# Optimization experiments

Measured on AMD Instinct MI355X. Metric: run time of the kernel, lower is better.

## Reference

```python
import jax, jax.numpy as jnp
import numpy as np

LMAX_IN = 3
LMAX_OUT = 3
C = 64          # num_channel
H = 64          # num_channel_hidden
N_NODES = 2048
N_EDGES = 8192

# All coupled (l1, l2, l3) paths with |l1-l2| <= l3 <= min(l1+l2, lmax_out)
COMBS = [(l1, l2, l3)
         for l1 in range(LMAX_IN + 1)
         for l2 in range(LMAX_OUT + 1)
         for l3 in range(abs(l1 - l2), min(l1 + l2, LMAX_OUT) + 1)]
COUNTS = {l3: sum(1 for c in COMBS if c[2] == l3) for l3 in range(LMAX_OUT + 1)}

# Fixed coupling (Clebsch-Gordan-like) tensors for each path, shape (2l1+1, 2l2+1, 2l3+1).
# Deterministic constants (not trained / not differentiated), standing in for the
# e3nn CG coefficients used by InterEinsumTC.
_rng = np.random.RandomState(1234)
CG = [jnp.asarray((_rng.randn(2 * l1 + 1, 2 * l2 + 1, 2 * l3 + 1) * 0.2).astype(np.float32))
      for (l1, l2, l3) in COMBS]


def setup_inputs() -> dict:
    key = jax.random.key(0)
    ks = jax.random.split(key, 16)
    inp = {}
    for l in range(LMAX_OUT + 1):
        inp[f"x{l}"] = jax.random.normal(ks[l], (N_NODES, C, 2 * l + 1), dtype=jnp.float32)
        inp[f"y{l}"] = jax.random.normal(ks[4 + l], (N_EDGES, 2 * l + 1), dtype=jnp.float32)
        fan_in = C * COUNTS[l]
        inp[f"w_lin{l}"] = jax.random.normal(ks[8 + l], (fan_in, H), dtype=jnp.float32) / np.float32(np.sqrt(fan_in))
    inp["ws"] = jax.random.normal(ks[12], (N_EDGES, C * len(COMBS)), dtype=jnp.float32)
    inp["edge_index"] = jax.random.randint(ks[13], (2, N_EDGES), 0, N_NODES, dtype=jnp.int32)
    return inp


def _forward(x0, x1, x2, x3, y0, y1, y2, y3, ws, w_lin0, w_lin1, w_lin2, w_lin3, edge_index):
    xs = (x0, x1, x2, x3)
    ys = (y0, y1, y2, y3)
    wl = (w_lin0, w_lin1, w_lin2, w_lin3)
    src, dst = edge_index[0], edge_index[1]
    # per-edge gather of node features for every input degree
    xg = [x[src] for x in xs]                      # [E, C, 2l1+1]
    buf = {l3: [] for l3 in range(LMAX_OUT + 1)}
    for i, (l1, l2, l3) in enumerate(COMBS):
        # tensor-product contraction: [E, C, 2l3+1]
        out = jnp.einsum('lmn,ecl,em->ecn', CG[i], xg[l1], ys[l2])
        w = ws[:, i * C:(i + 1) * C][:, :, None]   # [E, C, 1] per-path per-channel weight
        buf[l3].append(w * out)
    res = []
    for l3 in range(LMAX_OUT + 1):
        m_ji = jnp.concatenate(buf[l3], axis=1)    # [E, C*count_l3, 2l3+1]
        m_i = jax.ops.segment_sum(m_ji, dst, num_segments=N_NODES)  # scatter-sum -> [N, C*count, 2l3+1]
        res.append(jnp.einsum('ncm,ch->nhm', m_i, wl[l3]))          # per-l3 linear -> [N, H, 2l3+1]
    return tuple(res)


def reference(x0, x1, x2, x3, y0, y1, y2, y3, ws, w_lin0, w_lin1, w_lin2, w_lin3, edge_index):
    return _forward(x0, x1, x2, x3, y0, y1, y2, y3, ws,
                    w_lin0, w_lin1, w_lin2, w_lin3, edge_index)
```

## Files before the change

kernel.cpp:

```cpp
#include <hip/hip_runtime.h>
#include <hip/hip_bf16.h>
#include <cmath>
#include <cstdint>

#define NNODES 2048
#define NEDGES 8192
#define NCH 64
#define NHID 64
#define NPATH 34
#define NTASK (NPATH * NCH)
#define CGTOT 3436
#define MROW 9984
#define TTOT2 888
#define EBLK 8

#define MI_BYTES ((size_t)NNODES * MROW * 2)
#define XT_BYTES ((size_t)NNODES * 16 * NCH * 2)
#define OFF_OFF  (MI_BYTES)
#define CUR_OFF  (OFF_OFF + 2052 * 4)
#define PACK_OFF (CUR_OFF + 2048 * 4)
#define ORD_OFF  (PACK_OFF + 8192 * 4)
#define XT_OFF   (ORD_OFF + 2048 * 4)
#define CGP_OFF  (XT_OFF + XT_BYTES)
#define CGP_FLOATS (TTOT2 * 9)

typedef __attribute__((ext_vector_type(8))) short short8;
typedef __attribute__((ext_vector_type(4))) float floatx4;

struct PathTables {
  int l1[NPATH], l2[NPATH], l3[NPATH];
  int cg_off[NPATH], t_off2[NPATH], rank[NPATH];
  int gpaths[2][20], gnp[2], gbase[2], glen[2];
  int cg_total, ttot2, npaths;
};

constexpr PathTables make_tables() {
  PathTables tb{};
  int np = 0;
  for (int a = 0; a < 4; ++a)
    for (int b = 0; b < 4; ++b) {
      int lo = a > b ? a - b : b - a;
      int hi = a + b < 3 ? a + b : 3;
      for (int c = lo; c <= hi; ++c) { tb.l1[np] = a; tb.l2[np] = b; tb.l3[np] = c; ++np; }
    }
  int cg = 0;
  int cnt[4] = {0, 0, 0, 0};
  for (int i = 0; i < np; ++i) {
    tb.cg_off[i] = cg; tb.rank[i] = cnt[tb.l3[i]]++;
    cg += (2 * tb.l1[i] + 1) * (2 * tb.l2[i] + 1) * (2 * tb.l3[i] + 1);
  }
  int tt2 = 0;
  for (int g = 0; g < 2; ++g) {
    tb.gbase[g] = tt2;
    for (int i = 0; i < np; ++i) {
      int gi = (tb.l3[i] == 0 || tb.l3[i] == 3) ? 0 : 1;
      if (gi != g) continue;
      tb.gpaths[g][tb.gnp[g]++] = i;
      tb.t_off2[i] = tt2;
      int d1 = 2 * tb.l1[i] + 1, d3 = 2 * tb.l3[i] + 1;
      tt2 += ((d1 * d3 + 7) / 8) * 8;
    }
    tb.glen[g] = tt2 - tb.gbase[g];
  }
  tb.cg_total = cg; tb.ttot2 = tt2; tb.npaths = np;
  return tb;
}

constexpr PathTables H_TB = make_tables();
static_assert(H_TB.npaths == NPATH, "npaths");
static_assert(H_TB.cg_total == CGTOT, "cgtot");
static_assert(H_TB.ttot2 == TTOT2, "ttot2");
static_assert(H_TB.gnp[0] == 14 && H_TB.gnp[1] == 20, "gnp");
static_assert(H_TB.gbase[1] == 432 && H_TB.glen[1] == 456, "gsplit");

__constant__ PathTables d_tb = make_tables();

namespace {
struct MT19937 {
  uint32_t mt[624]; int mti; bool has_g; double gval;
  void seed(uint32_t s) {
    for (int i = 0; i < 624; ++i) { mt[i] = s; s = 1812433253u * (s ^ (s >> 30)) + (uint32_t)i + 1u; }
    mti = 624; has_g = false; gval = 0.0;
  }
  uint32_t next() {
    if (mti >= 624) {
      for (int i = 0; i < 624; ++i) {
        uint32_t y = (mt[i] & 0x80000000u) | (mt[(i + 1) % 624] & 0x7fffffffu);
        mt[i] = mt[(i + 397) % 624] ^ (y >> 1) ^ ((y & 1u) ? 0x9908b0dfu : 0u);
      }
      mti = 0;
    }
    uint32_t y = mt[mti++];
    y ^= y >> 11; y ^= (y << 7) & 0x9d2c5680u; y ^= (y << 15) & 0xefc60000u; y ^= y >> 18;
    return y;
  }
  double rdbl() {
    uint32_t a = next() >> 5, b = next() >> 6;
    return ((double)a * 67108864.0 + (double)b) / 9007199254740992.0;
  }
  double gauss() {
    if (has_g) { has_g = false; return gval; }
    double x1, x2, r2;
    do {
      x1 = 2.0 * rdbl() - 1.0;
      x2 = 2.0 * rdbl() - 1.0;
      r2 = x1 * x1 + x2 * x2;
    } while (r2 >= 1.0 || r2 == 0.0);
    double f = std::sqrt(-2.0 * std::log(r2) / r2);
    gval = f * x1; has_g = true;
    return f * x2;
  }
};

float host_pack[CGP_FLOATS];
float* g_cg_dev = nullptr;
bool g_cg_ok = false;

struct CGInit {
  CGInit() {
    static float cg[CGTOT];
    MT19937 g; g.seed(1234u);
    int idx = 0;
    for (int i = 0; i < NPATH; ++i) {
      int d1 = 2 * H_TB.l1[i] + 1, d2 = 2 * H_TB.l2[i] + 1, d3 = 2 * H_TB.l3[i] + 1;
      int sz = d1 * d2 * d3;
      for (int k = 0; k < sz; ++k) cg[idx++] = (float)(g.gauss() * 0.2);
    }
    const int ybase[4] = {0, 1, 4, 9};
    for (int k = 0; k < CGP_FLOATS; ++k) host_pack[k] = 0.f;
    for (int i = 0; i < NPATH; ++i) {
      int d1 = 2 * H_TB.l1[i] + 1, d2 = 2 * H_TB.l2[i] + 1, d3 = 2 * H_TB.l3[i] + 1;
      for (int l = 0; l < d1; ++l)
        for (int n3 = 0; n3 < d3; ++n3) {
          int tt2 = H_TB.t_off2[i] + l * d3 + n3;
          for (int m = 0; m < d2; ++m)
            host_pack[tt2 * 8 + m] = cg[H_TB.cg_off[i] + l * d2 * d3 + m * d3 + n3];
          host_pack[TTOT2 * 8 + tt2] = (float)ybase[H_TB.l2[i]];
        }
    }
    (void)hipHostRegister(host_pack, sizeof(host_pack), hipHostRegisterDefault);
    void* p = nullptr;
    if (hipMalloc(&p, sizeof(host_pack)) == hipSuccess && p) {
      if (hipMemcpy(p, host_pack, sizeof(host_pack), hipMemcpyHostToDevice) == hipSuccess) {
        float back = -1.f;
        if (hipMemcpy(&back, (float*)p + (CGP_FLOATS - 1), sizeof(float),
                      hipMemcpyDeviceToHost) == hipSuccess && back == host_pack[CGP_FLOATS - 1]) {
          g_cg_dev = (float*)p;
          g_cg_ok = true;
        }
      }
    }
  }
} cg_init_instance;
}

__device__ __forceinline__ float bf2f(unsigned short u) {
  union { unsigned int i; float f; } v; v.i = ((unsigned int)u) << 16; return v.f;
}
__device__ __forceinline__ unsigned short f2bf(float f) {
  __hip_bfloat16 h = __float2bfloat16(f);
  union { __hip_bfloat16 h; unsigned short u; } v; v.h = h; return v.u;
}

__global__ __launch_bounds__(1024) void scan_kernel(
    const int* __restrict__ edge_index, int* __restrict__ off, int* __restrict__ cursor,
    int* __restrict__ order)
{
  __shared__ int ldeg[NNODES];
  __shared__ int csum[1024];
  __shared__ int hist[64];
  const int t = threadIdx.x;
  for (int i = t; i < NNODES; i += 1024) ldeg[i] = 0;
  __syncthreads();
  const int* __restrict__ dsts = edge_index + NEDGES;
  for (int e = t; e < NEDGES; e += 1024) atomicAdd(&ldeg[dsts[e]], 1);
  __syncthreads();
  const int l0 = ldeg[2 * t], l1 = ldeg[2 * t + 1];
  const int s = l0 + l1;
  csum[t] = s;
  __syncthreads();
  for (int o = 1; o < 1024; o <<= 1) {
    int v = (t >= o) ? csum[t - o] : 0;
    __syncthreads();
    csum[t] += v;
    __syncthreads();
  }
  int run = csum[t] - s;
  off[2 * t] = run; cursor[2 * t] = run;
  off[2 * t + 1] = run + l0; cursor[2 * t + 1] = run + l0;
  if (t == 0) off[NNODES] = NEDGES;
  if (t < 64) hist[t] = 0;
  __syncthreads();
  for (int i = t; i < NNODES; i += 1024) {
    int d = ldeg[i]; d = d > 63 ? 63 : d;
    atomicAdd(&hist[63 - d], 1);
  }
  __syncthreads();
  if (t == 0) { int r2 = 0; for (int b = 0; b < 64; ++b) { int c = hist[b]; hist[b] = r2; r2 += c; } }
  __syncthreads();
  for (int i = t; i < NNODES; i += 1024) {
    int d = ldeg[i]; d = d > 63 ? 63 : d;
    int pos = atomicAdd(&hist[63 - d], 1);
    order[pos] = i;
  }
}

__global__ __launch_bounds__(256) void fill_xt_kernel(
    const int* __restrict__ edge_index, int* __restrict__ cursor, int* __restrict__ pack,
    const float* __restrict__ x0, const float* __restrict__ x1,
    const float* __restrict__ x2, const float* __restrict__ x3,
    __hip_bfloat16* __restrict__ xT)
{
  const int b = blockIdx.x;
  const int t = threadIdx.x;
  if (b < 32) {
    const int e = b * 256 + t;
    const int d = edge_index[NEDGES + e];
    const int s = edge_index[e];
    const int pos = atomicAdd(&cursor[d], 1);
    pack[pos] = e | (s << 13);
  } else {
    const int n = b - 32;
    for (int idx = t; idx < 1024; idx += 256) {
      const int j = idx >> 6, c = idx & 63;
      const float* src; int d1, m;
      if (j < 1)      { src = x0; d1 = 1; m = j; }
      else if (j < 4) { src = x1; d1 = 3; m = j - 1; }
      else if (j < 9) { src = x2; d1 = 5; m = j - 4; }
      else            { src = x3; d1 = 7; m = j - 9; }
      const float v = src[((size_t)n * NCH + c) * d1 + m];
      xT[((size_t)n * 16 + j) * NCH + c] = __float2bfloat16(v);
    }
  }
}

template <int D1, int D3>
__device__ __forceinline__ void tp_task_run(
    int wcol, int toff_l, int rank, int nb, const int* __restrict__ epk,
    const float (*Ts)[456], const float* __restrict__ ws,
    const unsigned short* __restrict__ xT,
    int n, bool first, __hip_bfloat16* __restrict__ m_out)
{
  constexpr int Kc = (D3 == 1) ? 256 : (D3 == 3) ? 576 : (D3 == 5) ? 704 : 640;
  constexpr int Rc = (D3 == 1) ? 0 : (D3 == 3) ? 256 : (D3 == 5) ? 1984 : 5504;
  constexpr int JB = (D1 == 1) ? 0 : (D1 == 3) ? 1 : (D1 == 5) ? 4 : 9;
  const int c = wcol & 63;

  float wv_[EBLK];
#pragma unroll
  for (int ei = 0; ei < EBLK; ++ei)
    wv_[ei] = (ei < nb) ? ws[(size_t)(epk[ei] & 8191) * NTASK + wcol] : 0.f;

  float acc[D3];
#pragma unroll
  for (int m = 0; m < D3; ++m) acc[m] = 0.f;

  for (int ei = 0; ei < nb; ++ei) {
    const int s = epk[ei] >> 13;
    const unsigned short* __restrict__ xr = xT + ((size_t)s * 16 + JB) * NCH + c;
    const float* __restrict__ Tp = &Ts[ei][toff_l];
    float u[D3];
#pragma unroll
    for (int m = 0; m < D3; ++m) u[m] = 0.f;
#pragma unroll
    for (int l = 0; l < D1; ++l) {
      const float xv = bf2f(xr[l * NCH]);
#pragma unroll
      for (int m = 0; m < D3; ++m) u[m] += xv * Tp[l * D3 + m];
    }
#pragma unroll
    for (int m = 0; m < D3; ++m) acc[m] += wv_[ei] * u[m];
  }

  __hip_bfloat16* mo = m_out + (size_t)n * MROW + Rc + rank * NCH + c;
  if (first) {
#pragma unroll
    for (int m = 0; m < D3; ++m) mo[m * Kc] = __float2bfloat16(acc[m]);
  } else {
#pragma unroll
    for (int m = 0; m < D3; ++m)
      mo[m * Kc] = __float2bfloat16(__bfloat162float(mo[m * Kc]) + acc[m]);
  }
}

__global__ __launch_bounds__(256) void tp_node_kernel(
    const float* __restrict__ y0, const float* __restrict__ y1,
    const float* __restrict__ y2, const float* __restrict__ y3,
    const float* __restrict__ ws, const unsigned short* __restrict__ xT,
    const float* __restrict__ cg_pack,
    const int* __restrict__ off, const int* __restrict__ pack,
    const int* __restrict__ order,
    __hip_bfloat16* __restrict__ m_out)
{
  __shared__ float Ts[EBLK][456];
  __shared__ float y_s[EBLK][18];
  __shared__ int epk[EBLK];

  const int bid = blockIdx.x;
  const int n = order[bid >> 1];
  const int g = bid & 1;
  const int t = threadIdx.x;
  const int beg = off[n];
  const int cnt = off[n + 1] - beg;
  const int gbase = d_tb.gbase[g];
  const int glen  = d_tb.glen[g];
  const int ntask = d_tb.gnp[g] << 6;
  const float* __restrict__ metaf = cg_pack + TTOT2 * 8;

  for (int base = 0; base == 0 || base < cnt; base += EBLK) {
    int nb = cnt - base;
    nb = nb < 0 ? 0 : (nb > EBLK ? EBLK : nb);
    if (t < nb) epk[t] = pack[beg + base + t];
    if (t >= 64 && t < 64 + 2 * EBLK) y_s[(t - 64) >> 1][16 + (t & 1)] = 0.f;
    __syncthreads();
    if (t < nb * 16) {
      const int ei = t >> 4, j = t & 15;
      const int e = epk[ei] & 8191;
      float v;
      if (j < 1)      v = y0[e];
      else if (j < 4) v = y1[e * 3 + (j - 1)];
      else if (j < 9) v = y2[e * 5 + (j - 4)];
      else            v = y3[e * 7 + (j - 9)];
      y_s[ei][j] = v;
    }
    __syncthreads();
    for (int ei = 0; ei < nb; ++ei) {
      for (int j = t; j < glen; j += 256) {
        const int tt2 = gbase + j;
        const float4 a = *(const float4*)(cg_pack + tt2 * 8);
        const float4 c4 = *(const float4*)(cg_pack + tt2 * 8 + 4);
        const int yb = (int)metaf[tt2];
        const float* yy = &y_s[ei][yb];
        Ts[ei][j] = a.x * yy[0] + a.y * yy[1] + a.z * yy[2] + a.w * yy[3]
                  + c4.x * yy[4] + c4.y * yy[5] + c4.z * yy[6] + c4.w * yy[7];
      }
    }
    __syncthreads();

    const bool first = (base == 0);
    for (int k = 0; k * 256 + t < ntask; ++k) {
      const int tl = k * 256 + t;
      const int i = d_tb.gpaths[g][tl >> 6];
      const int wcol = (i << 6) | (tl & 63);
      const int toff_l = d_tb.t_off2[i] - gbase;
      const int rk = d_tb.rank[i];
      const int code = d_tb.l1[i] * 4 + d_tb.l3[i];
      switch (code) {
        case  0: tp_task_run<1,1>(wcol, toff_l, rk, nb, epk, Ts, ws, xT, n, first, m_out); break;
        case  1: tp_task_run<1,3>(wcol, toff_l, rk, nb, epk, Ts, ws, xT, n, first, m_out); break;
        case  2: tp_task_run<1,5>(wcol, toff_l, rk, nb, epk, Ts, ws, xT, n, first, m_out); break;
        case  3: tp_task_run<1,7>(wcol, toff_l, rk, nb, epk, Ts, ws, xT, n, first, m_out); break;
        case  4: tp_task_run<3,1>(wcol, toff_l, rk, nb, epk, Ts, ws, xT, n, first, m_out); break;
        case  5: tp_task_run<3,3>(wcol, toff_l, rk, nb, epk, Ts, ws, xT, n, first, m_out); break;
        case  6: tp_task_run<3,5>(wcol, toff_l, rk, nb, epk, Ts, ws, xT, n, first, m_out); break;
        case  7: tp_task_run<3,7>(wcol, toff_l, rk, nb, epk, Ts, ws, xT, n, first, m_out); break;
        case  8: tp_task_run<5,1>(wcol, toff_l, rk, nb, epk, Ts, ws, xT, n, first, m_out); break;
        case  9: tp_task_run<5,3>(wcol, toff_l, rk, nb, epk, Ts, ws, xT, n, first, m_out); break;
        case 10: tp_task_run<5,5>(wcol, toff_l, rk, nb, epk, Ts, ws, xT, n, first, m_out); break;
        case 11: tp_task_run<5,7>(wcol, toff_l, rk, nb, epk, Ts, ws, xT, n, first, m_out); break;
        case 12: tp_task_run<7,1>(wcol, toff_l, rk, nb, epk, Ts, ws, xT, n, first, m_out); break;
        case 13: tp_task_run<7,3>(wcol, toff_l, rk, nb, epk, Ts, ws, xT, n, first, m_out); break;
        case 14: tp_task_run<7,5>(wcol, toff_l, rk, nb, epk, Ts, ws, xT, n, first, m_out); break;
        default: tp_task_run<7,7>(wcol, toff_l, rk, nb, epk, Ts, ws, xT, n, first, m_out); break;
      }
    }
    __syncthreads();
  }
}

template <int D3, int K, int ROFF>
__device__ __forceinline__ void lin_mfma_body(
    int blk, const unsigned short* __restrict__ mu, const float* __restrict__ wl,
    float* __restrict__ out, unsigned short (*A_s)[72], unsigned short (*W_s)[72])
{
  const int t = threadIdx.x;
  const int wv = t >> 6;
  const int lane = t & 63;
  const int idx16 = lane & 15;
  const int quad = lane >> 4;
  const int r0 = blk * 64;

  floatx4 acc[4] = {{0.f,0.f,0.f,0.f},{0.f,0.f,0.f,0.f},{0.f,0.f,0.f,0.f},{0.f,0.f,0.f,0.f}};

  for (int k0 = 0; k0 < K; k0 += 64) {
    for (int idx = t; idx < 512; idx += 256) {
      const int rr = idx >> 3, ck = (idx & 7) * 8;
      const int r = r0 + rr;
      const int nn = r / D3, mm = r - nn * D3;
      const uint4 v = *(const uint4*)(mu + (size_t)nn * MROW + ROFF + mm * K + k0 + ck);
      *(uint4*)&A_s[rr][ck] = v;
    }
    {
      const int h = t & 63, kg = t >> 6;
      unsigned short tmp[16];
#pragma unroll
      for (int j = 0; j < 16; ++j)
        tmp[j] = f2bf(wl[(size_t)(k0 + kg * 16 + j) * 64 + h]);
      *(uint4*)&W_s[h][kg * 16]     = *(const uint4*)&tmp[0];
      *(uint4*)&W_s[h][kg * 16 + 8] = *(const uint4*)&tmp[8];
    }
    __syncthreads();
#pragma unroll
    for (int ks = 0; ks < 2; ++ks) {
      const int kb = ks * 32 + quad * 8;
      const short8 af = *(const short8*)&A_s[wv * 16 + idx16][kb];
#pragma unroll
      for (int nt = 0; nt < 4; ++nt) {
        const short8 bf = *(const short8*)&W_s[nt * 16 + idx16][kb];
        acc[nt] = __builtin_amdgcn_mfma_f32_16x16x32_bf16(af, bf, acc[nt], 0, 0, 0);
      }
    }
    __syncthreads();
  }

#pragma unroll
  for (int nt = 0; nt < 4; ++nt) {
    const int h = nt * 16 + idx16;
#pragma unroll
    for (int r = 0; r < 4; ++r) {
      const int row = r0 + wv * 16 + quad * 4 + r;
      const int nn = row / D3, mm = row - nn * D3;
      out[((size_t)nn * NHID + h) * D3 + mm] = acc[nt][r];
    }
  }
}

__global__ __launch_bounds__(256) void lin_fused_kernel(
    const unsigned short* __restrict__ mu,
    const float* __restrict__ wl0, const float* __restrict__ wl1,
    const float* __restrict__ wl2, const float* __restrict__ wl3,
    float* __restrict__ out)
{
  __shared__ unsigned short A_s[64][72];
  __shared__ unsigned short W_s[64][72];
  const int b = blockIdx.x;
  if (b < 32)       lin_mfma_body<1, 256, 0>   (b,       mu, wl0, out,           A_s, W_s);
  else if (b < 128) lin_mfma_body<3, 576, 256> (b - 32,  mu, wl1, out + 131072,  A_s, W_s);
  else if (b < 288) lin_mfma_body<5, 704, 1984>(b - 128, mu, wl2, out + 524288,  A_s, W_s);
  else              lin_mfma_body<7, 640, 5504>(b - 288, mu, wl3, out + 1179648, A_s, W_s);
}

extern "C" void kernel_launch(void* const* d_in, const int* in_sizes, int n_in,
                              void* d_out, int out_size, void* d_ws, size_t ws_size,
                              hipStream_t stream) {
  const float* x0  = (const float*)d_in[0];
  const float* y0  = (const float*)d_in[1];
  const float* wl0 = (const float*)d_in[2];
  const float* x1  = (const float*)d_in[3];
  const float* y1  = (const float*)d_in[4];
  const float* wl1 = (const float*)d_in[5];
  const float* x2  = (const float*)d_in[6];
  const float* y2  = (const float*)d_in[7];
  const float* wl2 = (const float*)d_in[8];
  const float* x3  = (const float*)d_in[9];
  const float* y3  = (const float*)d_in[10];
  const float* wl3 = (const float*)d_in[11];
  const float* ws  = (const float*)d_in[12];
  const int* edge_index = (const int*)d_in[13];
  float* out = (float*)d_out;

  __hip_bfloat16* m_i = (__hip_bfloat16*)d_ws;
  int* csr_off = (int*)((char*)d_ws + OFF_OFF);
  int* cursor  = (int*)((char*)d_ws + CUR_OFF);
  int* pack    = (int*)((char*)d_ws + PACK_OFF);
  int* order   = (int*)((char*)d_ws + ORD_OFF);
  __hip_bfloat16* xT = (__hip_bfloat16*)((char*)d_ws + XT_OFF);

  const float* cg_pack;
  if (g_cg_ok) {
    cg_pack = g_cg_dev;
  } else {
    float* cg_ws = (float*)((char*)d_ws + CGP_OFF);
    hipMemcpyAsync(cg_ws, host_pack, sizeof(host_pack), hipMemcpyHostToDevice, stream);
    cg_pack = cg_ws;
  }

  scan_kernel<<<1, 1024, 0, stream>>>(edge_index, csr_off, cursor, order);
  fill_xt_kernel<<<32 + NNODES, 256, 0, stream>>>(edge_index, cursor, pack,
                                                  x0, x1, x2, x3, xT);
  tp_node_kernel<<<2 * NNODES, 256, 0, stream>>>(y0, y1, y2, y3, ws,
                                                 (const unsigned short*)xT, cg_pack,
                                                 csr_off, pack, order, m_i);
  lin_fused_kernel<<<512, 256, 0, stream>>>((const unsigned short*)m_i,
                                            wl0, wl1, wl2, wl3, out);
}
```

Baseline: 234.7 us.

## Stage gathered source features in LDS and prefetch per-path edge weights

Each edge block now copies the bf16 source-node feature rows into shared memory with one coalesced 8-byte load per thread, so the per-task inner loop reads x from LDS instead of doing scattered global bf16 loads. The per-edge ws weights are software-prefetched one task iteration ahead into registers to hide global latency. The CG/y precompute loop is also reordered so each thread loads the CG coefficients once and reuses them across all edges in the block. This adds 16KB of LDS and extra registers, which may lower occupancy.

```diff
diff --git a/kernel.cpp b/kernel.cpp
--- a/kernel.cpp
+++ b/kernel.cpp
@@ -236,35 +236,29 @@
 
 template <int D1, int D3>
 __device__ __forceinline__ void tp_task_run(
-    int wcol, int toff_l, int rank, int nb, const int* __restrict__ epk,
-    const float (*Ts)[456], const float* __restrict__ ws,
-    const unsigned short* __restrict__ xT,
+    int c, int toff_l, int rank, int nb,
+    const float (*Ts)[456], const unsigned short* xs, const float* wv_,
     int n, bool first, __hip_bfloat16* __restrict__ m_out)
 {
   constexpr int Kc = (D3 == 1) ? 256 : (D3 == 3) ? 576 : (D3 == 5) ? 704 : 640;
   constexpr int Rc = (D3 == 1) ? 0 : (D3 == 3) ? 256 : (D3 == 5) ? 1984 : 5504;
   constexpr int JB = (D1 == 1) ? 0 : (D1 == 3) ? 1 : (D1 == 5) ? 4 : 9;
-  const int c = wcol & 63;
-
-  float wv_[EBLK];
-#pragma unroll
-  for (int ei = 0; ei < EBLK; ++ei)
-    wv_[ei] = (ei < nb) ? ws[(size_t)(epk[ei] & 8191) * NTASK + wcol] : 0.f;
 
   float acc[D3];
 #pragma unroll
   for (int m = 0; m < D3; ++m) acc[m] = 0.f;
 
-  for (int ei = 0; ei < nb; ++ei) {
-    const int s = epk[ei] >> 13;
-    const unsigned short* __restrict__ xr = xT + ((size_t)s * 16 + JB) * NCH + c;
-    const float* __restrict__ Tp = &Ts[ei][toff_l];
+#pragma unroll
+  for (int ei = 0; ei < EBLK; ++ei) {
+    if (ei >= nb) break;
+    const unsigned short* xr = xs + (ei * 16 + JB) * 64 + c;
+    const float* Tp = &Ts[ei][toff_l];
     float u[D3];
 #pragma unroll
     for (int m = 0; m < D3; ++m) u[m] = 0.f;
 #pragma unroll
     for (int l = 0; l < D1; ++l) {
-      const float xv = bf2f(xr[l * NCH]);
+      const float xv = bf2f(xr[l * 64]);
 #pragma unroll
       for (int m = 0; m < D3; ++m) u[m] += xv * Tp[l * D3 + m];
     }
@@ -295,6 +289,7 @@
   __shared__ float Ts[EBLK][456];
   __shared__ float y_s[EBLK][18];
   __shared__ int epk[EBLK];
+  __shared__ unsigned short xs[EBLK][16][64];
 
   const int bid = blockIdx.x;
   const int n = order[bid >> 1];
@@ -323,13 +318,25 @@
       else            v = y3[e * 7 + (j - 9)];
       y_s[ei][j] = v;
     }
-    __syncthreads();
-    for (int ei = 0; ei < nb; ++ei) {
-      for (int j = t; j < glen; j += 256) {
-        const int tt2 = gbase + j;
-        const float4 a = *(const float4*)(cg_pack + tt2 * 8);
-        const float4 c4 = *(const float4*)(cg_pack + tt2 * 8 + 4);
-        const int yb = (int)metaf[tt2];
+    {
+      uint2 tmp[EBLK];
+#pragma unroll
+      for (int ei = 0; ei < EBLK; ++ei) {
+        const int s = (epk[ei] >> 13) & 2047;
+        const uint2* __restrict__ src = (const uint2*)(xT + ((size_t)s << 10));
+        if (ei < nb) tmp[ei] = src[t];
+      }
+#pragma unroll
+      for (int ei = 0; ei < EBLK; ++ei)
+        if (ei < nb) *((uint2*)(&xs[ei][0][0]) + t) = tmp[ei];
+    }
+    __syncthreads();
+    for (int j = t; j < glen; j += 256) {
+      const int tt2 = gbase + j;
+      const float4 a = *(const float4*)(cg_pack + tt2 * 8);
+      const float4 c4 = *(const float4*)(cg_pack + tt2 * 8 + 4);
+      const int yb = (int)metaf[tt2];
+      for (int ei = 0; ei < nb; ++ei) {
         const float* yy = &y_s[ei][yb];
         Ts[ei][j] = a.x * yy[0] + a.y * yy[1] + a.z * yy[2] + a.w * yy[3]
                   + c4.x * yy[4] + c4.y * yy[5] + c4.z * yy[6] + c4.w * yy[7];
@@ -338,30 +345,51 @@
     __syncthreads();
 
     const bool first = (base == 0);
+    const int c = t & 63;
+    float wcur[EBLK], wnxt[EBLK];
+    if (t < ntask) {
+      const int i0 = d_tb.gpaths[g][t >> 6];
+      const int wc0 = (i0 << 6) | (t & 63);
+#pragma unroll
+      for (int ei = 0; ei < EBLK; ++ei)
+        wcur[ei] = (ei < nb) ? ws[(size_t)(epk[ei] & 8191) * NTASK + wc0] : 0.f;
+    }
     for (int k = 0; k * 256 + t < ntask; ++k) {
       const int tl = k * 256 + t;
+      const int tln = tl + 256;
+      const bool more = tln < ntask;
+      if (more) {
+        const int in = d_tb.gpaths[g][tln >> 6];
+        const int wcn = (in << 6) | (tln & 63);
+#pragma unroll
+        for (int ei = 0; ei < EBLK; ++ei)
+          wnxt[ei] = (ei < nb) ? ws[(size_t)(epk[ei] & 8191) * NTASK + wcn] : 0.f;
+      }
       const int i = d_tb.gpaths[g][tl >> 6];
-      const int wcol = (i << 6) | (tl & 63);
       const int toff_l = d_tb.t_off2[i] - gbase;
       const int rk = d_tb.rank[i];
       const int code = d_tb.l1[i] * 4 + d_tb.l3[i];
       switch (code) {
-        case  0: tp_task_run<1,1>(wcol, toff_l, rk, nb, epk, Ts, ws, xT, n, first, m_out); break;
-        case  1: tp_task_run<1,3>(wcol, toff_l, rk, nb, epk, Ts, ws, xT, n, first, m_out); break;
-        case  2: tp_task_run<1,5>(wcol, toff_l, rk, nb, epk, Ts, ws, xT, n, first, m_out); break;
-        case  3: tp_task_run<1,7>(wcol, toff_l, rk, nb, epk, Ts, ws, xT, n, first, m_out); break;
-        case  4: tp_task_run<3,1>(wcol, toff_l, rk, nb, epk, Ts, ws, xT, n, first, m_out); break;
-        case  5: tp_task_run<3,3>(wcol, toff_l, rk, nb, epk, Ts, ws, xT, n, first, m_out); break;
-        case  6: tp_task_run<3,5>(wcol, toff_l, rk, nb, epk, Ts, ws, xT, n, first, m_out); break;
-        case  7: tp_task_run<3,7>(wcol, toff_l, rk, nb, epk, Ts, ws, xT, n, first, m_out); break;
-        case  8: tp_task_run<5,1>(wcol, toff_l, rk, nb, epk, Ts, ws, xT, n, first, m_out); break;
-        case  9: tp_task_run<5,3>(wcol, toff_l, rk, nb, epk, Ts, ws, xT, n, first, m_out); break;
-        case 10: tp_task_run<5,5>(wcol, toff_l, rk, nb, epk, Ts, ws, xT, n, first, m_out); break;
-        case 11: tp_task_run<5,7>(wcol, toff_l, rk, nb, epk, Ts, ws, xT, n, first, m_out); break;
-        case 12: tp_task_run<7,1>(wcol, toff_l, rk, nb, epk, Ts, ws, xT, n, first, m_out); break;
-        case 13: tp_task_run<7,3>(wcol, toff_l, rk, nb, epk, Ts, ws, xT, n, first, m_out); break;
-        case 14: tp_task_run<7,5>(wcol, toff_l, rk, nb, epk, Ts, ws, xT, n, first, m_out); break;
-        default: tp_task_run<7,7>(wcol, toff_l, rk, nb, epk, Ts, ws, xT, n, first, m_out); break;
+        case  0: tp_task_run<1,1>(c, toff_l, rk, nb, Ts, &xs[0][0][0], wcur, n, first, m_out); break;
+        case  1: tp_task_run<1,3>(c, toff_l, rk, nb, Ts, &xs[0][0][0], wcur, n, first, m_out); break;
+        case  2: tp_task_run<1,5>(c, toff_l, rk, nb, Ts, &xs[0][0][0], wcur, n, first, m_out); break;
+        case  3: tp_task_run<1,7>(c, toff_l, rk, nb, Ts, &xs[0][0][0], wcur, n, first, m_out); break;
+        case  4: tp_task_run<3,1>(c, toff_l, rk, nb, Ts, &xs[0][0][0], wcur, n, first, m_out); break;
+        case  5: tp_task_run<3,3>(c, toff_l, rk, nb, Ts, &xs[0][0][0], wcur, n, first, m_out); break;
+        case  6: tp_task_run<3,5>(c, toff_l, rk, nb, Ts, &xs[0][0][0], wcur, n, first, m_out); break;
+        case  7: tp_task_run<3,7>(c, toff_l, rk, nb, Ts, &xs[0][0][0], wcur, n, first, m_out); break;
+        case  8: tp_task_run<5,1>(c, toff_l, rk, nb, Ts, &xs[0][0][0], wcur, n, first, m_out); break;
+        case  9: tp_task_run<5,3>(c, toff_l, rk, nb, Ts, &xs[0][0][0], wcur, n, first, m_out); break;
+        case 10: tp_task_run<5,5>(c, toff_l, rk, nb, Ts, &xs[0][0][0], wcur, n, first, m_out); break;
+        case 11: tp_task_run<5,7>(c, toff_l, rk, nb, Ts, &xs[0][0][0], wcur, n, first, m_out); break;
+        case 12: tp_task_run<7,1>(c, toff_l, rk, nb, Ts, &xs[0][0][0], wcur, n, first, m_out); break;
+        case 13: tp_task_run<7,3>(c, toff_l, rk, nb, Ts, &xs[0][0][0], wcur, n, first, m_out); break;
+        case 14: tp_task_run<7,5>(c, toff_l, rk, nb, Ts, &xs[0][0][0], wcur, n, first, m_out); break;
+        default: tp_task_run<7,7>(c, toff_l, rk, nb, Ts, &xs[0][0][0], wcur, n, first, m_out); break;
+      }
+      if (more) {
+#pragma unroll
+        for (int ei = 0; ei < EBLK; ++ei) wcur[ei] = wnxt[ei];
       }
     }
     __syncthreads();
```

New measurement: 231.4 us, median of 2. Within noise of the previous version (-1.4%).

## Map one wave per node-group in tensor-product kernel with register-held edge data

Applied to the files above, without the earlier changes.

Restructures the tensor-product kernel so each 64-lane wave handles one (node, path-group) pair, with lanes as channels. Edge features are packed as bf16 pairs and held in registers, and the per-edge coupling table is stored edge-interleaved in LDS so it can be read as float4. ws loads are software-prefetched two paths ahead. Block-wide __syncthreads are replaced by wave-local lgkmcnt waits and the edge block shrinks to 4. The aim is to cut block synchronisation and redundant global loads. The cost is higher register pressure and a node-order remap that interleaves nodes across blocks.

```diff
diff --git a/kernel.cpp b/kernel.cpp
--- a/kernel.cpp
+++ b/kernel.cpp
@@ -12,10 +12,10 @@
 #define CGTOT 3436
 #define MROW 9984
 #define TTOT2 888
-#define EBLK 8
+#define EBLK 4
 
 #define MI_BYTES ((size_t)NNODES * MROW * 2)
-#define XT_BYTES ((size_t)NNODES * 16 * NCH * 2)
+#define XT_BYTES ((size_t)NNODES * 8 * NCH * 4)
 #define OFF_OFF  (MI_BYTES)
 #define CUR_OFF  (OFF_OFF + 2052 * 4)
 #define PACK_OFF (CUR_OFF + 2048 * 4)
@@ -126,7 +126,6 @@
       int sz = d1 * d2 * d3;
       for (int k = 0; k < sz; ++k) cg[idx++] = (float)(g.gauss() * 0.2);
     }
-    const int ybase[4] = {0, 1, 4, 9};
     for (int k = 0; k < CGP_FLOATS; ++k) host_pack[k] = 0.f;
     for (int i = 0; i < NPATH; ++i) {
       int d1 = 2 * H_TB.l1[i] + 1, d2 = 2 * H_TB.l2[i] + 1, d3 = 2 * H_TB.l3[i] + 1;
@@ -135,7 +134,7 @@
           int tt2 = H_TB.t_off2[i] + l * d3 + n3;
           for (int m = 0; m < d2; ++m)
             host_pack[tt2 * 8 + m] = cg[H_TB.cg_off[i] + l * d2 * d3 + m * d3 + n3];
-          host_pack[TTOT2 * 8 + tt2] = (float)ybase[H_TB.l2[i]];
+          host_pack[TTOT2 * 8 + tt2] = (float)H_TB.l2[i];
         }
     }
     (void)hipHostRegister(host_pack, sizeof(host_pack), hipHostRegisterDefault);
@@ -154,12 +153,15 @@
 } cg_init_instance;
 }
 
-__device__ __forceinline__ float bf2f(unsigned short u) {
-  union { unsigned int i; float f; } v; v.i = ((unsigned int)u) << 16; return v.f;
-}
 __device__ __forceinline__ unsigned short f2bf(float f) {
   __hip_bfloat16 h = __float2bfloat16(f);
   union { __hip_bfloat16 h; unsigned short u; } v; v.h = h; return v.u;
+}
+__device__ __forceinline__ float u2f(unsigned int u) {
+  union { unsigned int i; float f; } v; v.i = u; return v.f;
+}
+__device__ __forceinline__ void wave_fence() {
+  asm volatile("s_waitcnt lgkmcnt(0)" ::: "memory");
 }
 
 __global__ __launch_bounds__(1024) void scan_kernel(
@@ -209,7 +211,7 @@
     const int* __restrict__ edge_index, int* __restrict__ cursor, int* __restrict__ pack,
     const float* __restrict__ x0, const float* __restrict__ x1,
     const float* __restrict__ x2, const float* __restrict__ x3,
-    __hip_bfloat16* __restrict__ xT)
+    uint32_t* __restrict__ xTp)
 {
   const int b = blockIdx.x;
   const int t = threadIdx.x;
@@ -221,55 +223,56 @@
     pack[pos] = e | (s << 13);
   } else {
     const int n = b - 32;
-    for (int idx = t; idx < 1024; idx += 256) {
-      const int j = idx >> 6, c = idx & 63;
-      const float* src; int d1, m;
-      if (j < 1)      { src = x0; d1 = 1; m = j; }
-      else if (j < 4) { src = x1; d1 = 3; m = j - 1; }
-      else if (j < 9) { src = x2; d1 = 5; m = j - 4; }
-      else            { src = x3; d1 = 7; m = j - 9; }
-      const float v = src[((size_t)n * NCH + c) * d1 + m];
-      xT[((size_t)n * 16 + j) * NCH + c] = __float2bfloat16(v);
+    for (int idx = t; idx < 512; idx += 256) {
+      const int jp = idx >> 6, c = idx & 63;
+      float v[2];
+#pragma unroll
+      for (int h = 0; h < 2; ++h) {
+        const int j = 2 * jp + h;
+        const float* src; int d1, m;
+        if (j < 1)      { src = x0; d1 = 1; m = j; }
+        else if (j < 4) { src = x1; d1 = 3; m = j - 1; }
+        else if (j < 9) { src = x2; d1 = 5; m = j - 4; }
+        else            { src = x3; d1 = 7; m = j - 9; }
+        v[h] = src[((size_t)n * NCH + c) * d1 + m];
+      }
+      xTp[((size_t)n * 8 + jp) * NCH + c] =
+          (uint32_t)f2bf(v[0]) | ((uint32_t)f2bf(v[1]) << 16);
     }
   }
 }
 
 template <int D1, int D3>
-__device__ __forceinline__ void tp_task_run(
-    int wcol, int toff_l, int rank, int nb, const int* __restrict__ epk,
-    const float (*Ts)[456], const float* __restrict__ ws,
-    const unsigned short* __restrict__ xT,
-    int n, bool first, __hip_bfloat16* __restrict__ m_out)
+__device__ __forceinline__ void tp_path_run(
+    int c, int n, int nb, bool first, int toff, int rank,
+    const float (*Tsw)[EBLK], const uint32_t (&xq)[EBLK][8],
+    const float (&wv_)[EBLK], __hip_bfloat16* __restrict__ m_out)
 {
   constexpr int Kc = (D3 == 1) ? 256 : (D3 == 3) ? 576 : (D3 == 5) ? 704 : 640;
   constexpr int Rc = (D3 == 1) ? 0 : (D3 == 3) ? 256 : (D3 == 5) ? 1984 : 5504;
   constexpr int JB = (D1 == 1) ? 0 : (D1 == 3) ? 1 : (D1 == 5) ? 4 : 9;
-  const int c = wcol & 63;
-
-  float wv_[EBLK];
-#pragma unroll
-  for (int ei = 0; ei < EBLK; ++ei)
-    wv_[ei] = (ei < nb) ? ws[(size_t)(epk[ei] & 8191) * NTASK + wcol] : 0.f;
 
   float acc[D3];
 #pragma unroll
   for (int m = 0; m < D3; ++m) acc[m] = 0.f;
 
-  for (int ei = 0; ei < nb; ++ei) {
-    const int s = epk[ei] >> 13;
-    const unsigned short* __restrict__ xr = xT + ((size_t)s * 16 + JB) * NCH + c;
-    const float* __restrict__ Tp = &Ts[ei][toff_l];
-    float u[D3];
-#pragma unroll
-    for (int m = 0; m < D3; ++m) u[m] = 0.f;
-#pragma unroll
-    for (int l = 0; l < D1; ++l) {
-      const float xv = bf2f(xr[l * NCH]);
-#pragma unroll
-      for (int m = 0; m < D3; ++m) u[m] += xv * Tp[l * D3 + m];
-    }
-#pragma unroll
-    for (int m = 0; m < D3; ++m) acc[m] += wv_[ei] * u[m];
+#pragma unroll
+  for (int l = 0; l < D1; ++l) {
+    float wx[EBLK];
+#pragma unroll
+    for (int ei = 0; ei < EBLK; ++ei) {
+      const int j = JB + l;
+      const uint32_t q = xq[ei][j >> 1];
+      const uint32_t bits = (j & 1) ? (q & 0xffff0000u) : (q << 16);
+      wx[ei] = wv_[ei] * u2f(bits);
+    }
+    const float* tr = &Tsw[toff + l * D3][0];
+#pragma unroll
+    for (int m = 0; m < D3; ++m) {
+      const floatx4 t4 = *(const floatx4*)(tr + 4 * m);
+      acc[m] = fmaf(wx[3], t4[3], fmaf(wx[2], t4[2],
+               fmaf(wx[1], t4[1], fmaf(wx[0], t4[0], acc[m]))));
+    }
   }
 
   __hip_bfloat16* mo = m_out + (size_t)n * MROW + Rc + rank * NCH + c;
@@ -283,88 +286,134 @@
   }
 }
 
-__global__ __launch_bounds__(256) void tp_node_kernel(
+__global__ __launch_bounds__(256, 4) void tp_node_kernel(
     const float* __restrict__ y0, const float* __restrict__ y1,
     const float* __restrict__ y2, const float* __restrict__ y3,
-    const float* __restrict__ ws, const unsigned short* __restrict__ xT,
+    const float* __restrict__ ws, const uint32_t* __restrict__ xTp,
     const float* __restrict__ cg_pack,
     const int* __restrict__ off, const int* __restrict__ pack,
     const int* __restrict__ order,
     __hip_bfloat16* __restrict__ m_out)
 {
-  __shared__ float Ts[EBLK][456];
-  __shared__ float y_s[EBLK][18];
-  __shared__ int epk[EBLK];
-
-  const int bid = blockIdx.x;
-  const int n = order[bid >> 1];
-  const int g = bid & 1;
-  const int t = threadIdx.x;
+  __shared__ float Ts[4][456][EBLK];
+  __shared__ float y_w[4][128];
+
+  const int wv = threadIdx.x >> 6;
+  const int lane = threadIdx.x & 63;
+  const int wid = blockIdx.x * 4 + wv;
+  const int idx = wid >> 1;
+  const int g = wid & 1;
+  const int ridx = ((idx & 127) << 4) | (idx >> 7);
+  const int n = order[ridx];
   const int beg = off[n];
   const int cnt = off[n + 1] - beg;
   const int gbase = d_tb.gbase[g];
   const int glen  = d_tb.glen[g];
-  const int ntask = d_tb.gnp[g] << 6;
+  const int gnp   = d_tb.gnp[g];
   const float* __restrict__ metaf = cg_pack + TTOT2 * 8;
+  const float (*Tsw)[EBLK] = Ts[wv];
+  const int c = lane;
 
   for (int base = 0; base == 0 || base < cnt; base += EBLK) {
     int nb = cnt - base;
     nb = nb < 0 ? 0 : (nb > EBLK ? EBLK : nb);
-    if (t < nb) epk[t] = pack[beg + base + t];
-    if (t >= 64 && t < 64 + 2 * EBLK) y_s[(t - 64) >> 1][16 + (t & 1)] = 0.f;
-    __syncthreads();
-    if (t < nb * 16) {
-      const int ei = t >> 4, j = t & 15;
-      const int e = epk[ei] & 8191;
-      float v;
-      if (j < 1)      v = y0[e];
-      else if (j < 4) v = y1[e * 3 + (j - 1)];
-      else if (j < 9) v = y2[e * 5 + (j - 4)];
-      else            v = y3[e * 7 + (j - 9)];
-      y_s[ei][j] = v;
-    }
-    __syncthreads();
-    for (int ei = 0; ei < nb; ++ei) {
-      for (int j = t; j < glen; j += 256) {
-        const int tt2 = gbase + j;
-        const float4 a = *(const float4*)(cg_pack + tt2 * 8);
-        const float4 c4 = *(const float4*)(cg_pack + tt2 * 8 + 4);
-        const int yb = (int)metaf[tt2];
-        const float* yy = &y_s[ei][yb];
-        Ts[ei][j] = a.x * yy[0] + a.y * yy[1] + a.z * yy[2] + a.w * yy[3]
-                  + c4.x * yy[4] + c4.y * yy[5] + c4.z * yy[6] + c4.w * yy[7];
-      }
-    }
-    __syncthreads();
+
+    int pv = 0;
+    if (lane < nb) pv = pack[beg + base + lane];
+    int eix[EBLK], six[EBLK];
+#pragma unroll
+    for (int ei = 0; ei < EBLK; ++ei) {
+      const int p = __shfl(pv, ei);
+      eix[ei] = p & 8191;
+      six[ei] = p >> 13;
+    }
+
+    uint32_t xq[EBLK][8];
+#pragma unroll
+    for (int ei = 0; ei < EBLK; ++ei) {
+      const uint32_t* __restrict__ xb = xTp + ((size_t)six[ei] << 9) + c;
+#pragma unroll
+      for (int jp = 0; jp < 8; ++jp) xq[ei][jp] = xb[jp << 6];
+    }
+
+    wave_fence();
+#pragma unroll
+    for (int ss = 0; ss < 2; ++ss) {
+      const int s = lane + ss * 64;
+      const int ei = s >> 5, l2 = (s >> 3) & 3, m8 = s & 7;
+      const int e = __shfl(pv, ei) & 8191;
+      float v = 0.f;
+      if (m8 < 2 * l2 + 1) {
+        v = (l2 == 0) ? y0[e]
+          : (l2 == 1) ? y1[e * 3 + m8]
+          : (l2 == 2) ? y2[e * 5 + m8]
+          :             y3[e * 7 + m8];
+      }
+      y_w[wv][s] = v;
+    }
+    wave_fence();
+
+    for (int j = lane; j < glen; j += 64) {
+      const int tt2 = gbase + j;
+      const float4 a  = *(const float4*)(cg_pack + tt2 * 8);
+      const float4 c4 = *(const float4*)(cg_pack + tt2 * 8 + 4);
+      const int l2i = (int)metaf[tt2];
+      float4 tv;
+#pragma unroll
+      for (int ei = 0; ei < EBLK; ++ei) {
+        const float* yy = &y_w[wv][ei * 32 + l2i * 8];
+        const float4 ya = *(const float4*)yy;
+        const float4 yb = *(const float4*)(yy + 4);
+        const float t = a.x * ya.x + a.y * ya.y + a.z * ya.z + a.w * ya.w
+                      + c4.x * yb.x + c4.y * yb.y + c4.z * yb.z + c4.w * yb.w;
+        if (ei == 0) tv.x = t; else if (ei == 1) tv.y = t;
+        else if (ei == 2) tv.z = t; else tv.w = t;
+      }
+      *(float4*)&Ts[wv][j][0] = tv;
+    }
+    wave_fence();
 
     const bool first = (base == 0);
-    for (int k = 0; k * 256 + t < ntask; ++k) {
-      const int tl = k * 256 + t;
-      const int i = d_tb.gpaths[g][tl >> 6];
-      const int wcol = (i << 6) | (tl & 63);
-      const int toff_l = d_tb.t_off2[i] - gbase;
+    float w0[EBLK], w1[EBLK], w2[EBLK];
+#pragma unroll
+    for (int ei = 0; ei < EBLK; ++ei)
+      w0[ei] = (ei < nb) ? ws[(size_t)eix[ei] * NTASK + (d_tb.gpaths[g][0] << 6) + c] : 0.f;
+#pragma unroll
+    for (int ei = 0; ei < EBLK; ++ei)
+      w1[ei] = (ei < nb) ? ws[(size_t)eix[ei] * NTASK + (d_tb.gpaths[g][1] << 6) + c] : 0.f;
+
+    for (int k = 0; k < gnp; ++k) {
+      if (k + 2 < gnp) {
+        const int in = d_tb.gpaths[g][k + 2];
+#pragma unroll
+        for (int ei = 0; ei < EBLK; ++ei)
+          w2[ei] = (ei < nb) ? ws[(size_t)eix[ei] * NTASK + (in << 6) + c] : 0.f;
+      }
+      const int i = d_tb.gpaths[g][k];
+      const int toff = d_tb.t_off2[i] - gbase;
       const int rk = d_tb.rank[i];
       const int code = d_tb.l1[i] * 4 + d_tb.l3[i];
       switch (code) {
-        case  0: tp_task_run<1,1>(wcol, toff_l, rk, nb, epk, Ts, ws, xT, n, first, m_out); break;
-        case  1: tp_task_run<1,3>(wcol, toff_l, rk, nb, epk, Ts, ws, xT, n, first, m_out); break;
-        case  2: tp_task_run<1,5>(wcol, toff_l, rk, nb, epk, Ts, ws, xT, n, first, m_out); break;
-        case  3: tp_task_run<1,7>(wcol, toff_l, rk, nb, epk, Ts, ws, xT, n, first, m_out); break;
-        case  4: tp_task_run<3,1>(wcol, toff_l, rk, nb, epk, Ts, ws, xT, n, first, m_out); break;
-        case  5: tp_task_run<3,3>(wcol, toff_l, rk, nb, epk, Ts, ws, xT, n, first, m_out); break;
-        case  6: tp_task_run<3,5>(wcol, toff_l, rk, nb, epk, Ts, ws, xT, n, first, m_out); break;
-        case  7: tp_task_run<3,7>(wcol, toff_l, rk, nb, epk, Ts, ws, xT, n, first, m_out); break;
-        case  8: tp_task_run<5,1>(wcol, toff_l, rk, nb, epk, Ts, ws, xT, n, first, m_out); break;
-        case  9: tp_task_run<5,3>(wcol, toff_l, rk, nb, epk, Ts, ws, xT, n, first, m_out); break;
-        case 10: tp_task_run<5,5>(wcol, toff_l, rk, nb, epk, Ts, ws, xT, n, first, m_out); break;
-        case 11: tp_task_run<5,7>(wcol, toff_l, rk, nb, epk, Ts, ws, xT, n, first, m_out); break;
-        case 12: tp_task_run<7,1>(wcol, toff_l, rk, nb, epk, Ts, ws, xT, n, first, m_out); break;
-        case 13: tp_task_run<7,3>(wcol, toff_l, rk, nb, epk, Ts, ws, xT, n, first, m_out); break;
-        case 14: tp_task_run<7,5>(wcol, toff_l, rk, nb, epk, Ts, ws, xT, n, first, m_out); break;
-        default: tp_task_run<7,7>(wcol, toff_l, rk, nb, epk, Ts, ws, xT, n, first, m_out); break;
-      }
-    }
-    __syncthreads();
+        case  0: tp_path_run<1,1>(c, n, nb, first, toff, rk, Tsw, xq, w0, m_out); break;
+        case  1: tp_path_run<1,3>(c, n, nb, first, toff, rk, Tsw, xq, w0, m_out); break;
+        case  2: tp_path_run<1,5>(c, n, nb, first, toff, rk, Tsw, xq, w0, m_out); break;
+        case  3: tp_path_run<1,7>(c, n, nb, first, toff, rk, Tsw, xq, w0, m_out); break;
+        case  4: tp_path_run<3,1>(c, n, nb, first, toff, rk, Tsw, xq, w0, m_out); break;
+        case  5: tp_path_run<3,3>(c, n, nb, first, toff, rk, Tsw, xq, w0, m_out); break;
+        case  6: tp_path_run<3,5>(c, n, nb, first, toff, rk, Tsw, xq, w0, m_out); break;
+        case  7: tp_path_run<3,7>(c, n, nb, first, toff, rk, Tsw, xq, w0, m_out); break;
+        case  8: tp_path_run<5,1>(c, n, nb, first, toff, rk, Tsw, xq, w0, m_out); break;
+        case  9: tp_path_run<5,3>(c, n, nb, first, toff, rk, Tsw, xq, w0, m_out); break;
+        case 10: tp_path_run<5,5>(c, n, nb, first, toff, rk, Tsw, xq, w0, m_out); break;
+        case 11: tp_path_run<5,7>(c, n, nb, first, toff, rk, Tsw, xq, w0, m_out); break;
+        case 12: tp_path_run<7,1>(c, n, nb, first, toff, rk, Tsw, xq, w0, m_out); break;
+        case 13: tp_path_run<7,3>(c, n, nb, first, toff, rk, Tsw, xq, w0, m_out); break;
+        case 14: tp_path_run<7,5>(c, n, nb, first, toff, rk, Tsw, xq, w0, m_out); break;
+        default: tp_path_run<7,7>(c, n, nb, first, toff, rk, Tsw, xq, w0, m_out); break;
+      }
+#pragma unroll
+      for (int ei = 0; ei < EBLK; ++ei) { w0[ei] = w1[ei]; w1[ei] = w2[ei]; }
+    }
   }
 }
 
@@ -464,7 +513,7 @@
   int* cursor  = (int*)((char*)d_ws + CUR_OFF);
   int* pack    = (int*)((char*)d_ws + PACK_OFF);
   int* order   = (int*)((char*)d_ws + ORD_OFF);
-  __hip_bfloat16* xT = (__hip_bfloat16*)((char*)d_ws + XT_OFF);
+  uint32_t* xTp = (uint32_t*)((char*)d_ws + XT_OFF);
 
   const float* cg_pack;
   if (g_cg_ok) {
@@ -477,10 +526,9 @@
 
   scan_kernel<<<1, 1024, 0, stream>>>(edge_index, csr_off, cursor, order);
   fill_xt_kernel<<<32 + NNODES, 256, 0, stream>>>(edge_index, cursor, pack,
-                                                  x0, x1, x2, x3, xT);
-  tp_node_kernel<<<2 * NNODES, 256, 0, stream>>>(y0, y1, y2, y3, ws,
-                                                 (const unsigned short*)xT, cg_pack,
-                                                 csr_off, pack, order, m_i);
+                                                  x0, x1, x2, x3, xTp);
+  tp_node_kernel<<<1024, 256, 0, stream>>>(y0, y1, y2, y3, ws, xTp, cg_pack,
+                                           csr_off, pack, order, m_i);
   lin_fused_kernel<<<512, 256, 0, stream>>>((const unsigned short*)m_i,
                                             wl0, wl1, wl2, wl3, out);
 }
```

Result: slower. 389.0 us (+65.8%).
